# Kernel tuning notes

Measured on AMD Instinct MI355X. Metric: run time of the kernel, lower is better.

Reference implementation:

```python
import jax, jax.numpy as jnp
import numpy as np

N = 100000   # nodes per layer
E = 600000   # edges per block
FIN = 256    # raw feature dim
H = 128      # hidden_size
C = 47       # n_classes
L = 3        # num_layers = n_layers + 1
NOUT = 10000 # seed nodes
GEN_EPS = 1e-7
T = 1.0
LN_EPS = 1e-5


def setup_inputs() -> dict:
    key = jax.random.key(0)
    ks = jax.random.split(key, 10)
    return {
        "x": jax.random.normal(ks[0], (N, FIN), jnp.float32),
        "src": jax.random.randint(ks[1], (L - 1, E), 0, N),
        "dst": jax.random.randint(ks[2], (L - 1, E), 0, N),
        "node_map": jax.random.randint(ks[3], (L - 1, N), 0, N),
        "final_map": jax.random.randint(ks[4], (NOUT,), 0, N),
        "enc_w": jax.random.normal(ks[5], (FIN, H), jnp.float32) * 0.05,
        "enc_b": jnp.zeros((H,), jnp.float32),
        "gcn_w": jax.random.normal(ks[6], (L, H, H), jnp.float32) * 0.05,
        "gcn_b": jnp.zeros((L, H), jnp.float32),
        "ln_g": jnp.ones((L, H), jnp.float32),
        "ln_b": jnp.zeros((L, H), jnp.float32),
        "pred_w": jax.random.normal(ks[7], (H, C), jnp.float32) * 0.05,
        "pred_b": jnp.zeros((C,), jnp.float32),
    }


def _layer_norm(h, g, b):
    mu = jnp.mean(h, axis=-1, keepdims=True)
    var = jnp.mean(jnp.square(h - mu), axis=-1, keepdims=True)
    return (h - mu) * jax.lax.rsqrt(var + LN_EPS) * g + b


def _gen_conv(h, src, dst, w, b):
    # GENConv, aggr='softmax', mlp_layers=1, no edge_attr, no msg_norm.
    m = jax.nn.relu(h[src]) + GEN_EPS                      # [E, H] messages
    # per-destination, per-feature segment softmax with temperature T
    mx = jax.ops.segment_max(m * T, dst, num_segments=N)   # [N, H]
    e = jnp.exp(m * T - mx[dst])                           # [E, H]
    denom = jax.ops.segment_sum(e, dst, num_segments=N)    # [N, H]
    alpha = e / (denom[dst] + 1e-16)
    agg = jax.ops.segment_sum(m * alpha, dst, num_segments=N)  # [N, H]
    return (agg + h) @ w + b                               # residual + Linear (MLP)


def reference(x, src, dst, node_map, final_map, enc_w, enc_b,
              gcn_w, gcn_b, ln_g, ln_b, pred_w, pred_b):
    h = x @ enc_w + enc_b                                  # node_features_encoder
    h = _gen_conv(h, src[0], dst[0], gcn_w[0], gcn_b[0])   # gcns[0] with block-0 edges
    for layer in range(1, L):                              # res+ block
        h2 = jax.nn.relu(_layer_norm(h, ln_g[layer - 1], ln_b[layer - 1]))
        # dropout is identity in eval mode (p applied with training=False)
        # gcns[layer] uses the edge_index set BEFORE this iteration's move
        h = _gen_conv(h2, src[layer - 1], dst[layer - 1],
                      gcn_w[layer], gcn_b[layer]) + h
        h = h[node_map[layer - 1]]                         # nf_move_layer_to gather
    h = jax.nn.relu(_layer_norm(h, ln_g[L - 1], ln_b[L - 1]))
    h = h @ pred_w + pred_b                                # node_pred_linear
    h = h[final_map]                                       # seed-node extraction
    return jax.nn.log_softmax(h, axis=-1)
```

## Files before the change

kernel.cpp:

```cpp
#include <hip/hip_runtime.h>
#include <hip/hip_bf16.h>
#include <hip/hip_fp16.h>

typedef unsigned short u16;
typedef unsigned int u32;

#define N_NODES 100000
#define N_EDGES 600000
#define FIN_D   256
#define HDIM    128
#define NCLS    47
#define NOUT_D  10000
#define NCHUNK  196
#define NP2     100352
#define PCH     4096
#define PNB     ((N_EDGES + PCH - 1) / PCH)

typedef short bf16x8 __attribute__((ext_vector_type(8)));
typedef float f32x4  __attribute__((ext_vector_type(4)));

__device__ __forceinline__ float bf2f(u16 u) {
    union { u32 i; float f; } v; v.i = ((u32)u) << 16; return v.f;
}
__device__ __forceinline__ u16 f2bf(float f) {
    __hip_bfloat16 h = __float2bfloat16(f);
    return *reinterpret_cast<u16*>(&h);
}
__device__ __forceinline__ float loadF(const void* p, size_t i, bool f32) {
    if (f32) return ((const float*)p)[i];
    return bf2f(((const u16*)p)[i]);
}
__device__ __forceinline__ float wave_sum(float v) {
    #pragma unroll
    for (int o = 32; o > 0; o >>= 1) v += __shfl_xor(v, o, 64);
    return v;
}
__device__ __forceinline__ float wave_max(float v) {
    #pragma unroll
    for (int o = 32; o > 0; o >>= 1) v = fmaxf(v, __shfl_xor(v, o, 64));
    return v;
}
__device__ __forceinline__ int wave_sum_i(int v) {
    #pragma unroll
    for (int o = 32; o > 0; o >>= 1) v += __shfl_xor(v, o, 64);
    return v;
}
__device__ __forceinline__ int block_excl_scan_256(int v, int* wsum) {
    int lane = threadIdx.x & 63, wv = threadIdx.x >> 6;
    int inc = v;
    #pragma unroll
    for (int off = 1; off < 64; off <<= 1) {
        int u = __shfl_up(inc, off, 64);
        if (lane >= off) inc += u;
    }
    if (lane == 63) wsum[wv] = inc;
    __syncthreads();
    if (threadIdx.x == 0) {
        int a = 0;
        #pragma unroll
        for (int w = 0; w < 4; ++w) { int t = wsum[w]; wsum[w] = a; a += t; }
    }
    __syncthreads();
    return inc - v + wsum[wv];
}

__global__ __launch_bounds__(256) void dtype_detect_kernel(
    const u16* __restrict__ x, int* __restrict__ flag)
{
    __shared__ int cnt;
    if (threadIdx.x == 0) cnt = 0;
    __syncthreads();
    int local = 0;
    for (int i = threadIdx.x; i < 65536; i += 256) {
        u32 e = (x[i] >> 7) & 0xFF;
        if (e >= 200) local++;
    }
    atomicAdd(&cnt, local);
    __syncthreads();
    if (threadIdx.x == 0) *flag = (cnt > 16) ? 1 : 0;
}

__global__ __launch_bounds__(256) void hist2_kernel(
    const int* __restrict__ dst, int* __restrict__ deg2, int egrid)
{
    int half = (blockIdx.x >= egrid) ? 1 : 0;
    int e = (blockIdx.x - half * egrid) * 256 + threadIdx.x;
    if (e < N_EDGES) atomicAdd(&deg2[half * NP2 + dst[half * N_EDGES + e]], 1);
}

__global__ __launch_bounds__(256) void csum2_kernel(
    const int* __restrict__ deg2, int* __restrict__ csum)
{
    __shared__ int ws[4];
    int half = (blockIdx.x >= NCHUNK) ? 1 : 0;
    int b = blockIdx.x - half * NCHUNK;
    int i0 = half * NP2 + b * 512 + threadIdx.x;
    int v = 0;
    if (b * 512 + threadIdx.x < N_NODES) v += deg2[i0];
    if (b * 512 + threadIdx.x + 256 < N_NODES) v += deg2[i0 + 256];
    v = wave_sum_i(v);
    int lane = threadIdx.x & 63, wv = threadIdx.x >> 6;
    if (lane == 0) ws[wv] = v;
    __syncthreads();
    if (threadIdx.x == 0)
        csum[blockIdx.x] = ws[0] + ws[1] + ws[2] + ws[3];
}

__global__ __launch_bounds__(256) void coff2_kernel(
    const int* __restrict__ csum, int* __restrict__ coff,
    int* __restrict__ bcur)
{
    __shared__ int wsum[4];
    int t = threadIdx.x;
    for (int h = 0; h < 2; ++h) {
        int v = (t < NCHUNK) ? csum[h * NCHUNK + t] : 0;
        int excl = block_excl_scan_256(v, wsum);
        if (t < NCHUNK) {
            coff[h * NCHUNK + t] = excl;
            bcur[(h * NCHUNK + t) * 16] = excl;
        }
        __syncthreads();
    }
}

__global__ __launch_bounds__(256) void scan2_kernel(
    const int* __restrict__ deg2, const int* __restrict__ coff,
    int* __restrict__ rp0, int* __restrict__ rp1)
{
    __shared__ int wsum[4];
    int half = (blockIdx.x >= NCHUNK) ? 1 : 0;
    int b = blockIdx.x - half * NCHUNK;
    const int* deg = deg2 + half * NP2;
    int* rp = half ? rp1 : rp0;
    int t = threadIdx.x;
    int i0 = b * 512 + 2 * t;
    int d0 = (i0 < N_NODES) ? deg[i0] : 0;
    int d1 = (i0 + 1 < N_NODES) ? deg[i0 + 1] : 0;
    int excl = block_excl_scan_256(d0 + d1, wsum);
    int base = coff[half * NCHUNK + b] + excl;
    if (i0 < N_NODES)     rp[i0] = base;
    if (i0 + 1 < N_NODES) rp[i0 + 1] = base + d0;
    if (b == 0 && t == 0) rp[N_NODES] = N_EDGES;
}

__global__ __launch_bounds__(256) void bucket_part_kernel(
    const int* __restrict__ src, const int* __restrict__ dst,
    const int* __restrict__ comp1,
    int* __restrict__ bcur, int2* __restrict__ tmp)
{
    __shared__ int hist[NCHUNK];
    __shared__ int base[NCHUNK];
    int half = (blockIdx.x >= PNB) ? 1 : 0;
    int b = blockIdx.x - half * PNB;
    int e0 = b * PCH;
    for (int i = threadIdx.x; i < NCHUNK; i += 256) hist[i] = 0;
    __syncthreads();

    int2 loc[16];
    #pragma unroll
    for (int t = 0; t < 16; ++t) {
        int e = e0 + t * 256 + threadIdx.x;
        loc[t].y = -1;
        if (e < N_EDGES) {
            int ge = half * N_EDGES + e;
            int d = dst[ge];
            int s = src[ge];
            if (half) s = comp1[s];
            loc[t] = make_int2(s, d);
            atomicAdd(&hist[d >> 9], 1);
        }
    }
    __syncthreads();
    for (int i = threadIdx.x; i < NCHUNK; i += 256) {
        int h = hist[i];
        base[i] = (h > 0) ? atomicAdd(&bcur[(half * NCHUNK + i) * 16], h) : 0;
        hist[i] = 0;
    }
    __syncthreads();
    #pragma unroll
    for (int t = 0; t < 16; ++t) {
        if (loc[t].y >= 0) {
            int bk = loc[t].y >> 9;
            int pos = base[bk] + atomicAdd(&hist[bk], 1);
            tmp[(size_t)half * N_EDGES + pos] = loc[t];
        }
    }
}

__global__ __launch_bounds__(256) void bucket_sort_kernel(
    const int2* __restrict__ tmp,
    const int* __restrict__ rp0, const int* __restrict__ rp1,
    const int* __restrict__ coff, const int* __restrict__ csum,
    int* __restrict__ ei0, int* __restrict__ ei1)
{
    __shared__ int cur[512];
    int half = (blockIdx.x >= NCHUNK) ? 1 : 0;
    int b = blockIdx.x - half * NCHUNK;
    const int* rp = half ? rp1 : rp0;
    int* ei = half ? ei1 : ei0;
    int n0 = b * 512;
    #pragma unroll
    for (int i = threadIdx.x; i < 512; i += 256) {
        int n = n0 + i;
        cur[i] = (n < N_NODES) ? rp[n] : 0;
    }
    __syncthreads();
    int beg = coff[half * NCHUNK + b];
    int end = beg + csum[half * NCHUNK + b];
    for (int i = beg + threadIdx.x; i < end; i += 256) {
        int2 p = tmp[(size_t)half * N_EDGES + i];
        int pos = atomicAdd(&cur[p.y & 511], 1);
        ei[pos] = p.x;
    }
}

__global__ __launch_bounds__(256) void pack_b_kernel(
    const void* __restrict__ enc_w, const void* __restrict__ gcn_w,
    const int* __restrict__ dt, u16* __restrict__ Bp)
{
    const bool f32 = (*dt != 0);
    int o = blockIdx.x * 256 + threadIdx.x;
    if (o >= 32768 + 3 * 16384) return;
    const void* srcp; size_t soff; int m;
    if (o < 32768) { srcp = enc_w; soff = 0; m = o; }
    else {
        int l = (o - 32768) >> 14;
        srcp = gcn_w; soff = (size_t)l * 16384; m = (o - 32768) & 16383;
    }
    int j    = m & 7;
    int lane = (m >> 3) & 63;
    int ct   = (m >> 9) & 7;
    int kidx = m >> 12;
    int k = kidx * 32 + (lane >> 4) * 8 + j;
    int n = ct * 16 + (lane & 15);
    Bp[o] = f2bf(loadF(srcp, soff + (size_t)k * HDIM + n, f32));
}

__global__ __launch_bounds__(256) void enc_gemm_kernel(
    const void* __restrict__ Araw, const u16* __restrict__ Bp,
    const void* __restrict__ bias, const int* __restrict__ dt,
    u16* __restrict__ OutBF)
{
    const bool f32 = (*dt != 0);
    const int tid  = threadIdx.x;
    const int w    = tid >> 6;
    const int lane = tid & 63;
    const int quad = lane >> 4;
    const int cl   = lane & 15;
    const int m0   = blockIdx.x * 64;
    int arow = m0 + w * 16 + cl;
    if (arow >= N_NODES) arow = N_NODES - 1;

    f32x4 acc[8];
    #pragma unroll
    for (int ct = 0; ct < 8; ++ct) acc[ct] = (f32x4){0.f, 0.f, 0.f, 0.f};

    #pragma unroll
    for (int kidx = 0; kidx < 8; ++kidx) {
        bf16x8 a;
        if (!f32) {
            a = *(const bf16x8*)((const u16*)Araw +
                 (size_t)arow * FIN_D + kidx * 32 + quad * 8);
        } else {
            const float* ap = (const float*)Araw +
                 (size_t)arow * FIN_D + kidx * 32 + quad * 8;
            float4 v0 = *(const float4*)ap;
            float4 v1 = *(const float4*)(ap + 4);
            u32 p0 = (u32)f2bf(v0.x) | ((u32)f2bf(v0.y) << 16);
            u32 p1 = (u32)f2bf(v0.z) | ((u32)f2bf(v0.w) << 16);
            u32 p2 = (u32)f2bf(v1.x) | ((u32)f2bf(v1.y) << 16);
            u32 p3 = (u32)f2bf(v1.z) | ((u32)f2bf(v1.w) << 16);
            union { u32 u[4]; bf16x8 v; } cv;
            cv.u[0] = p0; cv.u[1] = p1; cv.u[2] = p2; cv.u[3] = p3;
            a = cv.v;
        }
        const u16* bb = Bp + ((size_t)(kidx * 8) * 64 + lane) * 8;
        #pragma unroll
        for (int ct = 0; ct < 8; ++ct) {
            bf16x8 b = *(const bf16x8*)(bb + (size_t)ct * 512);
            acc[ct] = __builtin_amdgcn_mfma_f32_16x16x32_bf16(a, b, acc[ct], 0, 0, 0);
        }
    }

    #pragma unroll
    for (int reg = 0; reg < 4; ++reg) {
        int grow = m0 + w * 16 + quad * 4 + reg;
        if (grow >= N_NODES) continue;
        #pragma unroll
        for (int ct = 0; ct < 8; ++ct) {
            int col = ct * 16 + cl;
            float v = acc[ct][reg] + loadF(bias, col, f32);
            OutBF[(size_t)grow * HDIM + col] = f2bf(v);
        }
    }
}

template<bool OWN_MAP>
__global__ __launch_bounds__(256) void agg_msg_kernel(
    const int* __restrict__ rp, const int* __restrict__ eidx,
    const u16* __restrict__ HBin, const int* __restrict__ own_map,
    u16* __restrict__ Amsg)
{
    int wave = threadIdx.x >> 6;
    int lane = threadIdx.x & 63;
    int n = blockIdx.x * 4 + wave;
    if (n >= N_NODES) return;
    const u32* HB32 = (const u32*)HBin;
    int nn = OWN_MAP ? own_map[n] : n;
    u32 own = HB32[(size_t)nn * 64 + lane];
    int beg = rp[n], end = rp[n + 1];
    float den0 = 0.f, den1 = 0.f, num0 = 0.f, num1 = 0.f;
    for (int j0 = beg; j0 < end; j0 += 8) {
        int cnt = end - j0; if (cnt > 8) cnt = 8;
        int ss[8];
        #pragma unroll
        for (int t = 0; t < 8; ++t) {
            int j = j0 + t;
            ss[t] = eidx[j < end ? j : end - 1];
        }
        u32 hh[8];
        #pragma unroll
        for (int t = 0; t < 8; ++t)
            hh[t] = HB32[(size_t)ss[t] * 64 + lane];
        #pragma unroll
        for (int t = 0; t < 8; ++t) {
            float valid = (t < cnt) ? 1.f : 0.f;
            float m0 = fmaxf(bf2f((u16)(hh[t] & 0xffff)), 0.f) + 1e-7f;
            float m1 = fmaxf(bf2f((u16)(hh[t] >> 16)),    0.f) + 1e-7f;
            float e0 = __expf(m0) * valid, e1 = __expf(m1) * valid;
            den0 += e0; num0 += m0 * e0;
            den1 += e1; num1 += m1 * e1;
        }
    }
    float a0 = num0 / (den0 + 1e-16f) + bf2f((u16)(own & 0xffff));
    float a1 = num1 / (den1 + 1e-16f) + bf2f((u16)(own >> 16));
    ((u32*)Amsg)[(size_t)n * 64 + lane] = (u32)f2bf(a0) | ((u32)f2bf(a1) << 16);
}

template<bool RES, bool OWN_MAP, bool WRITE_LN>
__global__ __launch_bounds__(256) void conv_gemm_kernel(
    const u16* __restrict__ Amsg, const int* __restrict__ own_map,
    const u16* __restrict__ Bp, int Bpbase,
    const void* __restrict__ bias, int biasoff,
    const __half* __restrict__ Resid,
    const void* __restrict__ lng, const void* __restrict__ lnb, int lnoff,
    const int* __restrict__ dt,
    __half* __restrict__ OutH, u16* __restrict__ HBout)
{
    const bool f32 = (*dt != 0);
    __shared__ u16 Bsh[16384];
    const int tid  = threadIdx.x;
    const int w    = tid >> 6;
    const int lane = tid & 63;
    const int quad = lane >> 4;
    const int cl   = lane & 15;
    const int m0   = blockIdx.x * 64;

    {
        const uint4* bsrc = (const uint4*)(Bp + Bpbase);
        uint4* bdst = (uint4*)Bsh;
        #pragma unroll
        for (int j = 0; j < 8; ++j)
            bdst[j * 256 + tid] = bsrc[j * 256 + tid];
    }

    int arow = m0 + w * 16 + cl;
    if (arow >= N_NODES) arow = N_NODES - 1;
    bf16x8 afr[4];
    #pragma unroll
    for (int kidx = 0; kidx < 4; ++kidx)
        afr[kidx] = *(const bf16x8*)(Amsg + (size_t)arow * HDIM + kidx * 32 + quad * 8);

    __syncthreads();

    f32x4 acc[8];
    #pragma unroll
    for (int ct = 0; ct < 8; ++ct) acc[ct] = (f32x4){0.f, 0.f, 0.f, 0.f};
    #pragma unroll
    for (int kidx = 0; kidx < 4; ++kidx) {
        const u16* bb = Bsh + ((size_t)(kidx * 8) * 64 + lane) * 8;
        #pragma unroll
        for (int ct = 0; ct < 8; ++ct) {
            bf16x8 b = *(const bf16x8*)(bb + (size_t)ct * 512);
            acc[ct] = __builtin_amdgcn_mfma_f32_16x16x32_bf16(afr[kidx], b, acc[ct], 0, 0, 0);
        }
    }

    #pragma unroll
    for (int reg = 0; reg < 4; ++reg) {
        int n = m0 + w * 16 + quad * 4 + reg;
        if (n >= N_NODES) continue;
        size_t rrow = 0;
        if (RES) rrow = (size_t)(OWN_MAP ? own_map[n] : n) * HDIM;
        float v[8];
        float s1 = 0.f, s2 = 0.f;
        #pragma unroll
        for (int ct = 0; ct < 8; ++ct) {
            int col = ct * 16 + cl;
            float x = acc[ct][reg] + loadF(bias, biasoff + col, f32);
            if (RES) x += __half2float(Resid[rrow + col]);
            v[ct] = x;
            OutH[(size_t)n * HDIM + col] = __float2half(x);
            s1 += x; s2 += x * x;
        }
        if (WRITE_LN) {
            #pragma unroll
            for (int o = 1; o < 16; o <<= 1) {
                s1 += __shfl_xor(s1, o, 64);
                s2 += __shfl_xor(s2, o, 64);
            }
            float mu = s1 * (1.0f / 128.0f);
            float var = s2 * (1.0f / 128.0f) - mu * mu;
            float rs = rsqrtf(fmaxf(var, 0.f) + 1e-5f);
            #pragma unroll
            for (int ct = 0; ct < 8; ++ct) {
                int col = ct * 16 + cl;
                float y = fmaxf((v[ct] - mu) * rs * loadF(lng, lnoff + col, f32)
                                + loadF(lnb, lnoff + col, f32), 0.f);
                HBout[(size_t)n * HDIM + col] = f2bf(y);
            }
        }
    }
}

__global__ __launch_bounds__(64) void final_head_kernel(
    const __half* __restrict__ Hsrc, const int* __restrict__ map1,
    const int* __restrict__ fmap,
    const void* __restrict__ g, const void* __restrict__ b, int goff,
    const void* __restrict__ pw, const void* __restrict__ pb,
    const int* __restrict__ dt, void* __restrict__ out)
{
    const bool f32 = (*dt != 0);
    __shared__ float sh[HDIM];
    int i = blockIdx.x;
    int lane = threadIdx.x;
    int jj = map1[fmap[i]];
    __half2 hv = *((const __half2*)(Hsrc + (size_t)jj * HDIM) + lane);
    float2 v = __half22float2(hv);
    float mu = wave_sum(v.x + v.y) * (1.0f / 128.0f);
    float d0 = v.x - mu, d1 = v.y - mu;
    float var = wave_sum(d0 * d0 + d1 * d1) * (1.0f / 128.0f);
    float rs = rsqrtf(var + 1e-5f);
    int f0 = lane * 2;
    sh[f0]     = fmaxf(d0 * rs * loadF(g, goff + f0, f32)     + loadF(b, goff + f0, f32),     0.0f);
    sh[f0 + 1] = fmaxf(d1 * rs * loadF(g, goff + f0 + 1, f32) + loadF(b, goff + f0 + 1, f32), 0.0f);
    __syncthreads();
    float acc = -1e30f;
    if (lane < NCLS) {
        acc = loadF(pb, lane, f32);
        #pragma unroll 4
        for (int k = 0; k < HDIM; ++k)
            acc = fmaf(sh[k], loadF(pw, k * NCLS + lane, f32), acc);
    }
    float mx = wave_max(acc);
    float ex = (lane < NCLS) ? __expf(acc - mx) : 0.0f;
    float sum = wave_sum(ex);
    if (lane < NCLS) {
        float r = acc - mx - logf(sum);
        if (f32) ((float*)out)[(size_t)i * NCLS + lane] = r;
        else     ((u16*)out)[(size_t)i * NCLS + lane] = f2bf(r);
    }
}

extern "C" void kernel_launch(void* const* d_in, const int* in_sizes, int n_in,
                              void* d_out, int out_size, void* d_ws, size_t ws_size,
                              hipStream_t stream) {
    const void* x       = d_in[0];
    const int* src      = (const int*)d_in[1];
    const int* dst      = (const int*)d_in[2];
    const int* node_map = (const int*)d_in[3];
    const int* fmap     = (const int*)d_in[4];
    const void* enc_w   = d_in[5];
    const void* enc_b   = d_in[6];
    const void* gcn_w   = d_in[7];
    const void* gcn_b   = d_in[8];
    const void* ln_g    = d_in[9];
    const void* ln_b    = d_in[10];
    const void* pred_w  = d_in[11];
    const void* pred_b  = d_in[12];

    char* ws = (char*)d_ws;
    const size_t szH = (size_t)N_NODES * HDIM * sizeof(u16);
    __half* Pa  = (__half*)ws;  ws += szH;
    __half* Pb  = (__half*)ws;  ws += szH;
    u16*   HBa  = (u16*)ws;     ws += szH;
    u16*   HBb  = (u16*)ws;     ws += szH;
    u16*   Amsg = (u16*)ws;     ws += szH;
    int*   FLAG = (int*)ws;     ws += 1024;
    u16*   Bp   = (u16*)ws;     ws += (size_t)(32768 + 3 * 16384) * 2 + 1024;
    int*  deg2  = (int*)ws;  ws += (size_t)2 * NP2 * 4;
    int*  rp0   = (int*)ws;  ws += (size_t)(N_NODES + 2) * 4;
    int*  rp1   = (int*)ws;  ws += (size_t)(N_NODES + 2) * 4;
    int*  ei0   = (int*)ws;  ws += (size_t)N_EDGES * 4;
    int*  ei1   = (int*)ws;  ws += (size_t)N_EDGES * 4;
    int2* tmp   = (int2*)ws; ws += (size_t)2 * N_EDGES * 8;
    int*  csum  = (int*)ws;  ws += 2048;
    int*  coff  = (int*)ws;  ws += 2048;
    int*  bcur  = (int*)ws;  ws += (size_t)2 * NCHUNK * 16 * 4 + 1024;

    dim3 blk(256);
    const int ggrid = (N_NODES + 63) / 64;
    const int egrid = (N_EDGES + 255) / 256;
    const int agrid = (N_NODES + 3) / 4;
    const int pgrid = (32768 + 3 * 16384 + 255) / 256;

    dtype_detect_kernel<<<1, blk, 0, stream>>>((const u16*)x, FLAG);
    pack_b_kernel<<<pgrid, blk, 0, stream>>>(enc_w, gcn_w, FLAG, Bp);

    hipMemsetAsync(deg2, 0, (size_t)2 * NP2 * 4, stream);
    hist2_kernel<<<2 * egrid, blk, 0, stream>>>(dst, deg2, egrid);
    csum2_kernel<<<2 * NCHUNK, blk, 0, stream>>>(deg2, csum);
    coff2_kernel<<<1, blk, 0, stream>>>(csum, coff, bcur);
    scan2_kernel<<<2 * NCHUNK, blk, 0, stream>>>(deg2, coff, rp0, rp1);
    bucket_part_kernel<<<2 * PNB, blk, 0, stream>>>(src, dst, node_map, bcur, tmp);
    bucket_sort_kernel<<<2 * NCHUNK, blk, 0, stream>>>(tmp, rp0, rp1, coff, csum,
                                                       ei0, ei1);

    enc_gemm_kernel<<<ggrid, blk, 0, stream>>>(x, Bp, enc_b, FLAG, HBa);

    agg_msg_kernel<false><<<agrid, blk, 0, stream>>>(rp0, ei0, HBa, nullptr, Amsg);
    conv_gemm_kernel<false, false, true><<<ggrid, blk, 0, stream>>>(
        Amsg, nullptr, Bp, 32768, gcn_b, 0, nullptr,
        ln_g, ln_b, 0, FLAG, Pa, HBb);

    agg_msg_kernel<false><<<agrid, blk, 0, stream>>>(rp0, ei0, HBb, nullptr, Amsg);
    conv_gemm_kernel<true, false, true><<<ggrid, blk, 0, stream>>>(
        Amsg, nullptr, Bp, 32768 + 16384, gcn_b, 128, Pa,
        ln_g, ln_b, 128, FLAG, Pb, HBa);

    agg_msg_kernel<true><<<agrid, blk, 0, stream>>>(rp1, ei1, HBa, node_map, Amsg);
    conv_gemm_kernel<true, true, false><<<ggrid, blk, 0, stream>>>(
        Amsg, node_map, Bp, 32768 + 2 * 16384, gcn_b, 256, Pb,
        ln_g, ln_b, 256, FLAG, Pa, nullptr);

    final_head_kernel<<<NOUT_D, dim3(64), 0, stream>>>(
        Pa, node_map + N_NODES, fmap, ln_g, ln_b, 256, pred_w, pred_b, FLAG,
        (void*)d_out);
}
```

Before: 628.8 us.

## Stage encoder weights in LDS, enlarge row tile, prefetch A operands

The encoder GEMM now copies the whole packed 256x128 bf16 weight matrix into shared memory with global_load_lds. Each block handles 256 rows instead of 64, with each wave doing four 16-row tiles. A fragments are software-pipelined: a triple buffer on the bf16 path and a double buffer on the fp32 path. The intent is to cut repeated global/L2 reads of B and hide latency on the memory-bound x stream, at the cost of 64KB LDS per block, more accumulator registers and fewer blocks.

```diff
diff --git a/kernel.cpp b/kernel.cpp
--- a/kernel.cpp
+++ b/kernel.cpp
@@ -236,61 +236,134 @@
     Bp[o] = f2bf(loadF(srcp, soff + (size_t)k * HDIM + n, f32));
 }
 
-__global__ __launch_bounds__(256) void enc_gemm_kernel(
+#define ELOADA(BUF, K)                                                         \
+    { _Pragma("unroll")                                                        \
+      for (int t = 0; t < 4; ++t)                                              \
+          BUF[t] = *(const bf16x8*)(baseA[t] + (K) * 32); }
+
+#define EK(K, B0, B1, B2)                                                      \
+    {                                                                          \
+        if ((K) + 2 < 8) ELOADA(B2, (K) + 2);                                  \
+        bf16x8 bf[8];                                                          \
+        _Pragma("unroll")                                                      \
+        for (int ct = 0; ct < 8; ++ct)                                         \
+            bf[ct] = *(const bf16x8*)(BshP + (K) * 4096 + ct * 512 + lane * 8);\
+        __builtin_amdgcn_sched_barrier(0);                                     \
+        _Pragma("unroll")                                                      \
+        for (int t = 0; t < 4; ++t)                                            \
+            _Pragma("unroll")                                                  \
+            for (int ct = 0; ct < 8; ++ct)                                     \
+                acc[t][ct] = __builtin_amdgcn_mfma_f32_16x16x32_bf16(          \
+                    B0[t], bf[ct], acc[t][ct], 0, 0, 0);                       \
+    }
+
+#define ELOADF(BUF, K)                                                         \
+    { _Pragma("unroll")                                                        \
+      for (int t = 0; t < 4; ++t) {                                            \
+          BUF[t][0] = *(const float4*)(baseAf[t] + (K) * 32);                  \
+          BUF[t][1] = *(const float4*)(baseAf[t] + (K) * 32 + 4);              \
+      } }
+
+#define EKF(K, RC, RN)                                                         \
+    {                                                                          \
+        if ((K) + 1 < 8) ELOADF(RN, (K) + 1);                                  \
+        bf16x8 av[4];                                                          \
+        _Pragma("unroll")                                                      \
+        for (int t = 0; t < 4; ++t) {                                          \
+            union { u32 u[4]; bf16x8 v; } cv;                                  \
+            cv.u[0] = (u32)f2bf(RC[t][0].x) | ((u32)f2bf(RC[t][0].y) << 16);   \
+            cv.u[1] = (u32)f2bf(RC[t][0].z) | ((u32)f2bf(RC[t][0].w) << 16);   \
+            cv.u[2] = (u32)f2bf(RC[t][1].x) | ((u32)f2bf(RC[t][1].y) << 16);   \
+            cv.u[3] = (u32)f2bf(RC[t][1].z) | ((u32)f2bf(RC[t][1].w) << 16);   \
+            av[t] = cv.v;                                                      \
+        }                                                                      \
+        bf16x8 bf[8];                                                          \
+        _Pragma("unroll")                                                      \
+        for (int ct = 0; ct < 8; ++ct)                                         \
+            bf[ct] = *(const bf16x8*)(BshP + (K) * 4096 + ct * 512 + lane * 8);\
+        __builtin_amdgcn_sched_barrier(0);                                     \
+        _Pragma("unroll")                                                      \
+        for (int t = 0; t < 4; ++t)                                            \
+            _Pragma("unroll")                                                  \
+            for (int ct = 0; ct < 8; ++ct)                                     \
+                acc[t][ct] = __builtin_amdgcn_mfma_f32_16x16x32_bf16(          \
+                    av[t], bf[ct], acc[t][ct], 0, 0, 0);                       \
+    }
+
+__global__ __launch_bounds__(256, 2) void enc_gemm_kernel(
     const void* __restrict__ Araw, const u16* __restrict__ Bp,
     const void* __restrict__ bias, const int* __restrict__ dt,
     u16* __restrict__ OutBF)
 {
+    __shared__ u16 Bsh[32768];
     const bool f32 = (*dt != 0);
     const int tid  = threadIdx.x;
     const int w    = tid >> 6;
     const int lane = tid & 63;
     const int quad = lane >> 4;
     const int cl   = lane & 15;
-    const int m0   = blockIdx.x * 64;
-    int arow = m0 + w * 16 + cl;
-    if (arow >= N_NODES) arow = N_NODES - 1;
-
-    f32x4 acc[8];
-    #pragma unroll
-    for (int ct = 0; ct < 8; ++ct) acc[ct] = (f32x4){0.f, 0.f, 0.f, 0.f};
-
-    #pragma unroll
-    for (int kidx = 0; kidx < 8; ++kidx) {
-        bf16x8 a;
-        if (!f32) {
-            a = *(const bf16x8*)((const u16*)Araw +
-                 (size_t)arow * FIN_D + kidx * 32 + quad * 8);
-        } else {
-            const float* ap = (const float*)Araw +
-                 (size_t)arow * FIN_D + kidx * 32 + quad * 8;
-            float4 v0 = *(const float4*)ap;
-            float4 v1 = *(const float4*)(ap + 4);
-            u32 p0 = (u32)f2bf(v0.x) | ((u32)f2bf(v0.y) << 16);
-            u32 p1 = (u32)f2bf(v0.z) | ((u32)f2bf(v0.w) << 16);
-            u32 p2 = (u32)f2bf(v1.x) | ((u32)f2bf(v1.y) << 16);
-            u32 p3 = (u32)f2bf(v1.z) | ((u32)f2bf(v1.w) << 16);
-            union { u32 u[4]; bf16x8 v; } cv;
-            cv.u[0] = p0; cv.u[1] = p1; cv.u[2] = p2; cv.u[3] = p3;
-            a = cv.v;
-        }
-        const u16* bb = Bp + ((size_t)(kidx * 8) * 64 + lane) * 8;
-        #pragma unroll
-        for (int ct = 0; ct < 8; ++ct) {
-            bf16x8 b = *(const bf16x8*)(bb + (size_t)ct * 512);
-            acc[ct] = __builtin_amdgcn_mfma_f32_16x16x32_bf16(a, b, acc[ct], 0, 0, 0);
-        }
-    }
-
-    #pragma unroll
-    for (int reg = 0; reg < 4; ++reg) {
-        int grow = m0 + w * 16 + quad * 4 + reg;
-        if (grow >= N_NODES) continue;
-        #pragma unroll
-        for (int ct = 0; ct < 8; ++ct) {
-            int col = ct * 16 + cl;
-            float v = acc[ct][reg] + loadF(bias, col, f32);
-            OutBF[(size_t)grow * HDIM + col] = f2bf(v);
+    const int m0   = blockIdx.x * 256;
+    const u16* BshP = &Bsh[0];
+
+    {
+        const char* gB = (const char*)Bp;
+        #pragma unroll
+        for (int i = 0; i < 16; ++i) {
+            size_t off = (size_t)w * 16384 + (size_t)i * 1024;
+            __builtin_amdgcn_global_load_lds(
+                (const __attribute__((address_space(1))) u32*)(gB + off + (size_t)lane * 16),
+                (__attribute__((address_space(3))) u32*)((char*)&Bsh[0] + off),
+                16, 0, 0);
+        }
+    }
+
+    int rows[4];
+    #pragma unroll
+    for (int t = 0; t < 4; ++t) {
+        int r = m0 + w * 64 + t * 16 + cl;
+        rows[t] = (r >= N_NODES) ? (N_NODES - 1) : r;
+    }
+
+    f32x4 acc[4][8];
+    #pragma unroll
+    for (int t = 0; t < 4; ++t)
+        #pragma unroll
+        for (int ct = 0; ct < 8; ++ct) acc[t][ct] = (f32x4){0.f, 0.f, 0.f, 0.f};
+
+    __syncthreads();
+
+    if (!f32) {
+        const u16* baseA[4];
+        #pragma unroll
+        for (int t = 0; t < 4; ++t)
+            baseA[t] = (const u16*)Araw + (size_t)rows[t] * FIN_D + quad * 8;
+        bf16x8 a0[4], a1[4], a2[4];
+        ELOADA(a0, 0); ELOADA(a1, 1);
+        EK(0, a0, a1, a2) EK(1, a1, a2, a0) EK(2, a2, a0, a1) EK(3, a0, a1, a2)
+        EK(4, a1, a2, a0) EK(5, a2, a0, a1) EK(6, a0, a1, a2) EK(7, a1, a2, a0)
+    } else {
+        const float* baseAf[4];
+        #pragma unroll
+        for (int t = 0; t < 4; ++t)
+            baseAf[t] = (const float*)Araw + (size_t)rows[t] * FIN_D + quad * 8;
+        float4 f0[4][2], f1[4][2];
+        ELOADF(f0, 0);
+        EKF(0, f0, f1) EKF(1, f1, f0) EKF(2, f0, f1) EKF(3, f1, f0)
+        EKF(4, f0, f1) EKF(5, f1, f0) EKF(6, f0, f1) EKF(7, f1, f0)
+    }
+
+    #pragma unroll
+    for (int t = 0; t < 4; ++t) {
+        #pragma unroll
+        for (int reg = 0; reg < 4; ++reg) {
+            int grow = m0 + w * 64 + t * 16 + quad * 4 + reg;
+            if (grow >= N_NODES) continue;
+            #pragma unroll
+            for (int ct = 0; ct < 8; ++ct) {
+                int col = ct * 16 + cl;
+                float v = acc[t][ct][reg] + loadF(bias, col, f32);
+                OutBF[(size_t)grow * HDIM + col] = f2bf(v);
+            }
         }
     }
 }
@@ -500,6 +573,7 @@
 
     dim3 blk(256);
     const int ggrid = (N_NODES + 63) / 64;
+    const int g256  = (N_NODES + 255) / 256;
     const int egrid = (N_EDGES + 255) / 256;
     const int agrid = (N_NODES + 3) / 4;
     const int pgrid = (32768 + 3 * 16384 + 255) / 256;
@@ -516,7 +590,7 @@
     bucket_sort_kernel<<<2 * NCHUNK, blk, 0, stream>>>(tmp, rp0, rp1, coff, csum,
                                                        ei0, ei1);
 
-    enc_gemm_kernel<<<ggrid, blk, 0, stream>>>(x, Bp, enc_b, FLAG, HBa);
+    enc_gemm_kernel<<<g256, blk, 0, stream>>>(x, Bp, enc_b, FLAG, HBa);
 
     agg_msg_kernel<false><<<agrid, blk, 0, stream>>>(rp0, ei0, HBa, nullptr, Amsg);
     conv_gemm_kernel<false, false, true><<<ggrid, blk, 0, stream>>>(
```

Result: no change. 622.3 us (-1.0%).

## Stage encoder GEMM through LDS with async double-buffered loads and parallel dtype detect

Applied to the files above, without the earlier changes.

The encoder GEMM now uses 512-thread blocks covering 256 rows each. It copies the packed weight matrix into LDS and double-buffers A tiles with global_load_lds, so the next K-chunk loads while MFMAs run on the current one. Each wave computes two 16-row tiles, which reuses the B fragments, at the cost of 128KB of dynamic LDS and one block per CU. The dtype detection kernel also spreads from a single block to 256 blocks using ballot and popcount. Its count now goes through a memset and global atomics, and each consumer checks the threshold itself.

```diff
diff --git a/kernel.cpp b/kernel.cpp
--- a/kernel.cpp
+++ b/kernel.cpp
@@ -67,17 +67,13 @@
 __global__ __launch_bounds__(256) void dtype_detect_kernel(
     const u16* __restrict__ x, int* __restrict__ flag)
 {
-    __shared__ int cnt;
-    if (threadIdx.x == 0) cnt = 0;
-    __syncthreads();
-    int local = 0;
-    for (int i = threadIdx.x; i < 65536; i += 256) {
-        u32 e = (x[i] >> 7) & 0xFF;
-        if (e >= 200) local++;
-    }
-    atomicAdd(&cnt, local);
-    __syncthreads();
-    if (threadIdx.x == 0) *flag = (cnt > 16) ? 1 : 0;
+    int i = blockIdx.x * 256 + threadIdx.x;
+    u32 e = (x[i] >> 7) & 0xFF;
+    unsigned long long b = __ballot(e >= 200);
+    if ((threadIdx.x & 63) == 0) {
+        int c = __popcll(b);
+        if (c) atomicAdd(&flag[1], c);
+    }
 }
 
 __global__ __launch_bounds__(256) void hist2_kernel(
@@ -218,7 +214,7 @@
     const void* __restrict__ enc_w, const void* __restrict__ gcn_w,
     const int* __restrict__ dt, u16* __restrict__ Bp)
 {
-    const bool f32 = (*dt != 0);
+    const bool f32 = (dt[1] > 16);
     int o = blockIdx.x * 256 + threadIdx.x;
     if (o >= 32768 + 3 * 16384) return;
     const void* srcp; size_t soff; int m;
@@ -236,61 +232,111 @@
     Bp[o] = f2bf(loadF(srcp, soff + (size_t)k * HDIM + n, f32));
 }
 
-__global__ __launch_bounds__(256) void enc_gemm_kernel(
+#define ENC_AB(BUF) (65536 + (BUF) * 32768)
+
+#define STAGE_A32(KC, BUF)                                                     \
+    { _Pragma("unroll")                                                        \
+      for (int i = 0; i < 4; ++i) {                                            \
+          int rowl = i * 64 + w * 8 + (lane >> 3);                             \
+          int gr = m0 + rowl; if (gr > N_NODES - 1) gr = N_NODES - 1;          \
+          __builtin_amdgcn_global_load_lds(                                    \
+              (const __attribute__((address_space(1))) u32*)((const char*)Araw \
+                  + (size_t)gr * 1024 + (KC) * 128 + (lane & 7) * 16),         \
+              (__attribute__((address_space(3))) u32*)(SH + ENC_AB(BUF)        \
+                  + i * 8192 + w * 1024), 16, 0, 0);                           \
+      } }
+
+#define STAGE_A16(KC, BUF)                                                     \
+    { _Pragma("unroll")                                                        \
+      for (int i = 0; i < 2; ++i) {                                            \
+          int rowl = i * 128 + w * 16 + (lane >> 2);                           \
+          int gr = m0 + rowl; if (gr > N_NODES - 1) gr = N_NODES - 1;          \
+          __builtin_amdgcn_global_load_lds(                                    \
+              (const __attribute__((address_space(1))) u32*)((const char*)Araw \
+                  + (size_t)gr * 512 + (KC) * 64 + (lane & 3) * 16),           \
+              (__attribute__((address_space(3))) u32*)(SH + ENC_AB(BUF)        \
+                  + i * 8192 + w * 1024), 16, 0, 0);                           \
+      } }
+
+__global__ __launch_bounds__(512, 1) void enc_gemm_kernel(
     const void* __restrict__ Araw, const u16* __restrict__ Bp,
     const void* __restrict__ bias, const int* __restrict__ dt,
     u16* __restrict__ OutBF)
 {
-    const bool f32 = (*dt != 0);
+    extern __shared__ char SH[];
+    const bool f32 = (dt[1] > 16);
     const int tid  = threadIdx.x;
     const int w    = tid >> 6;
     const int lane = tid & 63;
     const int quad = lane >> 4;
     const int cl   = lane & 15;
-    const int m0   = blockIdx.x * 64;
-    int arow = m0 + w * 16 + cl;
-    if (arow >= N_NODES) arow = N_NODES - 1;
-
-    f32x4 acc[8];
-    #pragma unroll
-    for (int ct = 0; ct < 8; ++ct) acc[ct] = (f32x4){0.f, 0.f, 0.f, 0.f};
-
-    #pragma unroll
-    for (int kidx = 0; kidx < 8; ++kidx) {
-        bf16x8 a;
+    const int m0   = blockIdx.x * 256;
+
+    #pragma unroll
+    for (int i = 0; i < 8; ++i) {
+        int off = i * 8192 + w * 1024;
+        __builtin_amdgcn_global_load_lds(
+            (const __attribute__((address_space(1))) u32*)((const char*)Bp + off + lane * 16),
+            (__attribute__((address_space(3))) u32*)(SH + off), 16, 0, 0);
+    }
+    if (!f32) { STAGE_A16(0, 0) } else { STAGE_A32(0, 0) }
+
+    f32x4 acc[2][8];
+    #pragma unroll
+    for (int t = 0; t < 2; ++t)
+        #pragma unroll
+        for (int ct = 0; ct < 8; ++ct) acc[t][ct] = (f32x4){0.f, 0.f, 0.f, 0.f};
+
+    const int rl0 = w * 32 + cl;
+    __syncthreads();
+
+    #pragma unroll
+    for (int k = 0; k < 8; ++k) {
+        const int cur = k & 1;
+        if (k < 7) {
+            if (!f32) { STAGE_A16((k + 1), ((k + 1) & 1)) }
+            else      { STAGE_A32((k + 1), ((k + 1) & 1)) }
+        }
+        bf16x8 av[2];
         if (!f32) {
-            a = *(const bf16x8*)((const u16*)Araw +
-                 (size_t)arow * FIN_D + kidx * 32 + quad * 8);
+            #pragma unroll
+            for (int t = 0; t < 2; ++t)
+                av[t] = *(const bf16x8*)(SH + ENC_AB(cur) + (rl0 + t * 16) * 64 + quad * 16);
         } else {
-            const float* ap = (const float*)Araw +
-                 (size_t)arow * FIN_D + kidx * 32 + quad * 8;
-            float4 v0 = *(const float4*)ap;
-            float4 v1 = *(const float4*)(ap + 4);
-            u32 p0 = (u32)f2bf(v0.x) | ((u32)f2bf(v0.y) << 16);
-            u32 p1 = (u32)f2bf(v0.z) | ((u32)f2bf(v0.w) << 16);
-            u32 p2 = (u32)f2bf(v1.x) | ((u32)f2bf(v1.y) << 16);
-            u32 p3 = (u32)f2bf(v1.z) | ((u32)f2bf(v1.w) << 16);
-            union { u32 u[4]; bf16x8 v; } cv;
-            cv.u[0] = p0; cv.u[1] = p1; cv.u[2] = p2; cv.u[3] = p3;
-            a = cv.v;
-        }
-        const u16* bb = Bp + ((size_t)(kidx * 8) * 64 + lane) * 8;
+            #pragma unroll
+            for (int t = 0; t < 2; ++t) {
+                const char* p = SH + ENC_AB(cur) + (rl0 + t * 16) * 128 + quad * 32;
+                float4 lo = *(const float4*)p;
+                float4 hi = *(const float4*)(p + 16);
+                union { u32 u[4]; bf16x8 v; } cv;
+                cv.u[0] = (u32)f2bf(lo.x) | ((u32)f2bf(lo.y) << 16);
+                cv.u[1] = (u32)f2bf(lo.z) | ((u32)f2bf(lo.w) << 16);
+                cv.u[2] = (u32)f2bf(hi.x) | ((u32)f2bf(hi.y) << 16);
+                cv.u[3] = (u32)f2bf(hi.z) | ((u32)f2bf(hi.w) << 16);
+                av[t] = cv.v;
+            }
+        }
         #pragma unroll
         for (int ct = 0; ct < 8; ++ct) {
-            bf16x8 b = *(const bf16x8*)(bb + (size_t)ct * 512);
-            acc[ct] = __builtin_amdgcn_mfma_f32_16x16x32_bf16(a, b, acc[ct], 0, 0, 0);
-        }
-    }
-
-    #pragma unroll
-    for (int reg = 0; reg < 4; ++reg) {
-        int grow = m0 + w * 16 + quad * 4 + reg;
-        if (grow >= N_NODES) continue;
-        #pragma unroll
-        for (int ct = 0; ct < 8; ++ct) {
-            int col = ct * 16 + cl;
-            float v = acc[ct][reg] + loadF(bias, col, f32);
-            OutBF[(size_t)grow * HDIM + col] = f2bf(v);
+            bf16x8 b = *(const bf16x8*)(SH + (size_t)k * 8192 + ct * 1024 + lane * 16);
+            acc[0][ct] = __builtin_amdgcn_mfma_f32_16x16x32_bf16(av[0], b, acc[0][ct], 0, 0, 0);
+            acc[1][ct] = __builtin_amdgcn_mfma_f32_16x16x32_bf16(av[1], b, acc[1][ct], 0, 0, 0);
+        }
+        __syncthreads();
+    }
+
+    #pragma unroll
+    for (int t = 0; t < 2; ++t) {
+        #pragma unroll
+        for (int reg = 0; reg < 4; ++reg) {
+            int grow = m0 + w * 32 + t * 16 + quad * 4 + reg;
+            if (grow >= N_NODES) continue;
+            #pragma unroll
+            for (int ct = 0; ct < 8; ++ct) {
+                int col = ct * 16 + cl;
+                float v = acc[t][ct][reg] + loadF(bias, col, f32);
+                OutBF[(size_t)grow * HDIM + col] = f2bf(v);
+            }
         }
     }
 }
@@ -347,7 +393,7 @@
     const int* __restrict__ dt,
     __half* __restrict__ OutH, u16* __restrict__ HBout)
 {
-    const bool f32 = (*dt != 0);
+    const bool f32 = (dt[1] > 16);
     __shared__ u16 Bsh[16384];
     const int tid  = threadIdx.x;
     const int w    = tid >> 6;
@@ -430,7 +476,7 @@
     const void* __restrict__ pw, const void* __restrict__ pb,
     const int* __restrict__ dt, void* __restrict__ out)
 {
-    const bool f32 = (*dt != 0);
+    const bool f32 = (dt[1] > 16);
     __shared__ float sh[HDIM];
     int i = blockIdx.x;
     int lane = threadIdx.x;
@@ -500,11 +546,13 @@
 
     dim3 blk(256);
     const int ggrid = (N_NODES + 63) / 64;
+    const int g256  = (N_NODES + 255) / 256;
     const int egrid = (N_EDGES + 255) / 256;
     const int agrid = (N_NODES + 3) / 4;
     const int pgrid = (32768 + 3 * 16384 + 255) / 256;
 
-    dtype_detect_kernel<<<1, blk, 0, stream>>>((const u16*)x, FLAG);
+    hipMemsetAsync(FLAG, 0, 64, stream);
+    dtype_detect_kernel<<<256, blk, 0, stream>>>((const u16*)x, FLAG);
     pack_b_kernel<<<pgrid, blk, 0, stream>>>(enc_w, gcn_w, FLAG, Bp);
 
     hipMemsetAsync(deg2, 0, (size_t)2 * NP2 * 4, stream);
@@ -516,7 +564,7 @@
     bucket_sort_kernel<<<2 * NCHUNK, blk, 0, stream>>>(tmp, rp0, rp1, coff, csum,
                                                        ei0, ei1);
 
-    enc_gemm_kernel<<<ggrid, blk, 0, stream>>>(x, Bp, enc_b, FLAG, HBa);
+    enc_gemm_kernel<<<g256, dim3(512), 131072, stream>>>(x, Bp, enc_b, FLAG, HBa);
 
     agg_msg_kernel<false><<<agrid, blk, 0, stream>>>(rp0, ei0, HBa, nullptr, Amsg);
     conv_gemm_kernel<false, false, true><<<ggrid, blk, 0, stream>>>(
```

After: 581.8 us. 7.5% less time.

## Stage encoder GEMM operands in LDS via direct global-to-LDS loads and parallelize dtype detection

Applied to the files above, without the earlier changes.

The encoder GEMM now processes 16 rows per block, with each wave computing 2 of the 8 column tiles. The full packed weight matrix and the A tile are loaded straight into LDS with global_load_lds, and the A rows use an XOR swizzle to avoid bank conflicts. This is meant to cut redundant per-wave global reads of B and improve memory-level parallelism, at the cost of 80KB of LDS per block and reloading all of B for every 16-row block. The dtype-detect kernel is also changed from a single block to a 256-block ballot and popcount reduction with an atomic counter, which removes a serial startup step.

```diff
diff --git a/kernel.cpp b/kernel.cpp
--- a/kernel.cpp
+++ b/kernel.cpp
@@ -19,6 +19,9 @@
 typedef short bf16x8 __attribute__((ext_vector_type(8)));
 typedef float f32x4  __attribute__((ext_vector_type(4)));
 
+#define GPTR(p) (const __attribute__((address_space(1))) u32*)(p)
+#define LPTR(p) (__attribute__((address_space(3))) u32*)(p)
+
 __device__ __forceinline__ float bf2f(u16 u) {
     union { u32 i; float f; } v; v.i = ((u32)u) << 16; return v.f;
 }
@@ -67,17 +70,13 @@
 __global__ __launch_bounds__(256) void dtype_detect_kernel(
     const u16* __restrict__ x, int* __restrict__ flag)
 {
-    __shared__ int cnt;
-    if (threadIdx.x == 0) cnt = 0;
-    __syncthreads();
-    int local = 0;
-    for (int i = threadIdx.x; i < 65536; i += 256) {
-        u32 e = (x[i] >> 7) & 0xFF;
-        if (e >= 200) local++;
-    }
-    atomicAdd(&cnt, local);
-    __syncthreads();
-    if (threadIdx.x == 0) *flag = (cnt > 16) ? 1 : 0;
+    int i = blockIdx.x * 256 + threadIdx.x;
+    u32 e = (x[i] >> 7) & 0xFF;
+    unsigned long long b = __ballot(e >= 200);
+    if ((threadIdx.x & 63) == 0) {
+        int c = __popcll(b);
+        if (c) atomicAdd(&flag[1], c);
+    }
 }
 
 __global__ __launch_bounds__(256) void hist2_kernel(
@@ -218,7 +217,7 @@
     const void* __restrict__ enc_w, const void* __restrict__ gcn_w,
     const int* __restrict__ dt, u16* __restrict__ Bp)
 {
-    const bool f32 = (*dt != 0);
+    const bool f32 = (dt[1] > 16);
     int o = blockIdx.x * 256 + threadIdx.x;
     if (o >= 32768 + 3 * 16384) return;
     const void* srcp; size_t soff; int m;
@@ -236,60 +235,88 @@
     Bp[o] = f2bf(loadF(srcp, soff + (size_t)k * HDIM + n, f32));
 }
 
-__global__ __launch_bounds__(256) void enc_gemm_kernel(
+__global__ __launch_bounds__(256, 2) void enc_gemm_kernel(
     const void* __restrict__ Araw, const u16* __restrict__ Bp,
     const void* __restrict__ bias, const int* __restrict__ dt,
     u16* __restrict__ OutBF)
 {
-    const bool f32 = (*dt != 0);
+    extern __shared__ char SH[];
+    const bool f32 = (dt[1] > 16);
     const int tid  = threadIdx.x;
     const int w    = tid >> 6;
     const int lane = tid & 63;
     const int quad = lane >> 4;
     const int cl   = lane & 15;
-    const int m0   = blockIdx.x * 64;
-    int arow = m0 + w * 16 + cl;
-    if (arow >= N_NODES) arow = N_NODES - 1;
-
-    f32x4 acc[8];
-    #pragma unroll
-    for (int ct = 0; ct < 8; ++ct) acc[ct] = (f32x4){0.f, 0.f, 0.f, 0.f};
-
-    #pragma unroll
-    for (int kidx = 0; kidx < 8; ++kidx) {
-        bf16x8 a;
-        if (!f32) {
-            a = *(const bf16x8*)((const u16*)Araw +
-                 (size_t)arow * FIN_D + kidx * 32 + quad * 8);
+    const int m0   = blockIdx.x * 16;
+
+    #pragma unroll
+    for (int i = 0; i < 16; ++i) {
+        int off = (w * 16 + i) * 1024;
+        __builtin_amdgcn_global_load_lds(
+            GPTR((const char*)Bp + off + lane * 16),
+            LPTR(SH + off), 16, 0, 0);
+    }
+    if (f32) {
+        #pragma unroll
+        for (int i = 0; i < 4; ++i) {
+            int row = w * 4 + i;
+            int src = (lane * 16) ^ ((row & 7) << 4);
+            __builtin_amdgcn_global_load_lds(
+                GPTR((const char*)Araw + (size_t)(m0 + row) * 1024 + src),
+                LPTR(SH + 65536 + row * 1024), 16, 0, 0);
+        }
+    } else {
+        #pragma unroll
+        for (int i = 0; i < 2; ++i) {
+            int r0 = (w * 2 + i) * 2;
+            int row = r0 + (lane >> 5);
+            int src = ((lane & 31) * 16) ^ ((row & 7) << 4);
+            __builtin_amdgcn_global_load_lds(
+                GPTR((const char*)Araw + (size_t)(m0 + row) * 512 + src),
+                LPTR(SH + 65536 + r0 * 512), 16, 0, 0);
+        }
+    }
+
+    f32x4 acc[2];
+    acc[0] = (f32x4){0.f, 0.f, 0.f, 0.f};
+    acc[1] = (f32x4){0.f, 0.f, 0.f, 0.f};
+    const int ct0 = w * 2;
+    const int swz = (cl & 7) << 4;
+
+    __syncthreads();
+
+    #pragma unroll
+    for (int k = 0; k < 8; ++k) {
+        bf16x8 av;
+        if (f32) {
+            const char* rb = SH + 65536 + cl * 1024;
+            int lo = (k * 128 + quad * 32) ^ swz;
+            float4 v0 = *(const float4*)(rb + lo);
+            float4 v1 = *(const float4*)(rb + (lo ^ 16));
+            union { u32 u[4]; bf16x8 v; } cv;
+            cv.u[0] = (u32)f2bf(v0.x) | ((u32)f2bf(v0.y) << 16);
+            cv.u[1] = (u32)f2bf(v0.z) | ((u32)f2bf(v0.w) << 16);
+            cv.u[2] = (u32)f2bf(v1.x) | ((u32)f2bf(v1.y) << 16);
+            cv.u[3] = (u32)f2bf(v1.z) | ((u32)f2bf(v1.w) << 16);
+            av = cv.v;
         } else {
-            const float* ap = (const float*)Araw +
-                 (size_t)arow * FIN_D + kidx * 32 + quad * 8;
-            float4 v0 = *(const float4*)ap;
-            float4 v1 = *(const float4*)(ap + 4);
-            u32 p0 = (u32)f2bf(v0.x) | ((u32)f2bf(v0.y) << 16);
-            u32 p1 = (u32)f2bf(v0.z) | ((u32)f2bf(v0.w) << 16);
-            u32 p2 = (u32)f2bf(v1.x) | ((u32)f2bf(v1.y) << 16);
-            u32 p3 = (u32)f2bf(v1.z) | ((u32)f2bf(v1.w) << 16);
-            union { u32 u[4]; bf16x8 v; } cv;
-            cv.u[0] = p0; cv.u[1] = p1; cv.u[2] = p2; cv.u[3] = p3;
-            a = cv.v;
-        }
-        const u16* bb = Bp + ((size_t)(kidx * 8) * 64 + lane) * 8;
-        #pragma unroll
-        for (int ct = 0; ct < 8; ++ct) {
-            bf16x8 b = *(const bf16x8*)(bb + (size_t)ct * 512);
-            acc[ct] = __builtin_amdgcn_mfma_f32_16x16x32_bf16(a, b, acc[ct], 0, 0, 0);
+            const char* rb = SH + 65536 + cl * 512;
+            av = *(const bf16x8*)(rb + ((k * 64 + quad * 16) ^ swz));
+        }
+        #pragma unroll
+        for (int c = 0; c < 2; ++c) {
+            bf16x8 b = *(const bf16x8*)(SH + k * 8192 + (ct0 + c) * 1024 + lane * 16);
+            acc[c] = __builtin_amdgcn_mfma_f32_16x16x32_bf16(av, b, acc[c], 0, 0, 0);
         }
     }
 
     #pragma unroll
     for (int reg = 0; reg < 4; ++reg) {
-        int grow = m0 + w * 16 + quad * 4 + reg;
-        if (grow >= N_NODES) continue;
-        #pragma unroll
-        for (int ct = 0; ct < 8; ++ct) {
-            int col = ct * 16 + cl;
-            float v = acc[ct][reg] + loadF(bias, col, f32);
+        int grow = m0 + quad * 4 + reg;
+        #pragma unroll
+        for (int c = 0; c < 2; ++c) {
+            int col = (ct0 + c) * 16 + cl;
+            float v = acc[c][reg] + loadF(bias, col, f32);
             OutBF[(size_t)grow * HDIM + col] = f2bf(v);
         }
     }
@@ -347,7 +374,7 @@
     const int* __restrict__ dt,
     __half* __restrict__ OutH, u16* __restrict__ HBout)
 {
-    const bool f32 = (*dt != 0);
+    const bool f32 = (dt[1] > 16);
     __shared__ u16 Bsh[16384];
     const int tid  = threadIdx.x;
     const int w    = tid >> 6;
@@ -430,7 +457,7 @@
     const void* __restrict__ pw, const void* __restrict__ pb,
     const int* __restrict__ dt, void* __restrict__ out)
 {
-    const bool f32 = (*dt != 0);
+    const bool f32 = (dt[1] > 16);
     __shared__ float sh[HDIM];
     int i = blockIdx.x;
     int lane = threadIdx.x;
@@ -500,11 +527,13 @@
 
     dim3 blk(256);
     const int ggrid = (N_NODES + 63) / 64;
+    const int g16   = (N_NODES + 15) / 16;
     const int egrid = (N_EDGES + 255) / 256;
     const int agrid = (N_NODES + 3) / 4;
     const int pgrid = (32768 + 3 * 16384 + 255) / 256;
 
-    dtype_detect_kernel<<<1, blk, 0, stream>>>((const u16*)x, FLAG);
+    hipMemsetAsync(FLAG, 0, 64, stream);
+    dtype_detect_kernel<<<256, blk, 0, stream>>>((const u16*)x, FLAG);
     pack_b_kernel<<<pgrid, blk, 0, stream>>>(enc_w, gcn_w, FLAG, Bp);
 
     hipMemsetAsync(deg2, 0, (size_t)2 * NP2 * 4, stream);
@@ -516,7 +545,7 @@
     bucket_sort_kernel<<<2 * NCHUNK, blk, 0, stream>>>(tmp, rp0, rp1, coff, csum,
                                                        ei0, ei1);
 
-    enc_gemm_kernel<<<ggrid, blk, 0, stream>>>(x, Bp, enc_b, FLAG, HBa);
+    enc_gemm_kernel<<<g16, blk, 81920, stream>>>(x, Bp, enc_b, FLAG, HBa);
 
     agg_msg_kernel<false><<<agrid, blk, 0, stream>>>(rp0, ei0, HBa, nullptr, Amsg);
     conv_gemm_kernel<false, false, true><<<ggrid, blk, 0, stream>>>(
```

Measured after the change: 575.3 us. -8.5%, faster.
